# Performance work log

Measured on AMD Instinct MI355X. Metric: run time of the kernel, lower is better.

## Reference

```python
import jax, jax.numpy as jnp
import numpy as np

B, LQ, LK, LKL = 4, 1024, 1024, 512
DX, H, DK = 1024, 16, 64
ALPHA = 0.5
NEG = -1e9
EPS = 1e-5


def setup_inputs() -> dict:
    key = jax.random.key(0)
    ks = jax.random.split(key, 24)
    s = 0.02
    inp = {
        "q": jax.random.normal(ks[0], (B, LQ, DX), jnp.float32),
        "k": jax.random.normal(ks[1], (B, LK, DX), jnp.float32),
        "v": jax.random.normal(ks[2], (B, LK, DX), jnp.float32),
        "kl": jax.random.normal(ks[3], (B, LKL, DX), jnp.float32),
        "vl": jax.random.normal(ks[4], (B, LKL, DX), jnp.float32),
        "pad_mask": jax.random.randint(ks[5], (B, LQ, LK), 0, 2).astype(bool),
        "pad_mask_l": jax.random.randint(ks[6], (B, LQ, LKL), 0, 2).astype(bool),
        "wq_w": jax.random.normal(ks[7], (DX, H * DK), jnp.float32) * s,
        "wq_b": jnp.zeros((H * DK,), jnp.float32),
        "wk_w": jax.random.normal(ks[8], (DX, H * DK), jnp.float32) * s,
        "wk_b": jnp.zeros((H * DK,), jnp.float32),
        "wv_w": jax.random.normal(ks[9], (DX, H * DK), jnp.float32) * s,
        "wv_b": jnp.zeros((H * DK,), jnp.float32),
        "wkl_w": jax.random.normal(ks[10], (DX, H * DK), jnp.float32) * s,
        "wkl_b": jnp.zeros((H * DK,), jnp.float32),
        "wvl_w": jax.random.normal(ks[11], (DX, H * DK), jnp.float32) * s,
        "wvl_b": jnp.zeros((H * DK,), jnp.float32),
        "wo_w": jax.random.normal(ks[12], (H * DK, DX), jnp.float32) * s,
        "wo_b": jnp.zeros((DX,), jnp.float32),
        "ln_g": jnp.ones((DX,), jnp.float32),
        "ln_b": jnp.zeros((DX,), jnp.float32),
    }
    return inp


def _heads(x, w, b, L):
    # (B, L, DX) @ (DX, H*DK) -> (B, H, L, DK)
    y = x @ w + b
    return y.reshape(B, L, H, DK).transpose(0, 2, 1, 3)


def _attn(qh, kh, vh, mask):
    # qh: (B,H,Lq,D), kh/vh: (B,H,Lk,D), mask: (B,Lq,Lk) bool (True = masked)
    scores = jnp.einsum("bhqd,bhkd->bhqk", qh, kh) / np.sqrt(DK).astype(np.float32)
    scores = jnp.where(mask[:, None, :, :], NEG, scores)
    attn = jax.nn.softmax(scores, axis=-1)
    out = jnp.einsum("bhqk,bhkd->bhqd", attn, vh)
    return out, attn


def reference(q, k, v, kl, vl, pad_mask, pad_mask_l,
              wq_w, wq_b, wk_w, wk_b, wv_w, wv_b,
              wkl_w, wkl_b, wvl_w, wvl_b, wo_w, wo_b, ln_g, ln_b):
    X = q
    qh = _heads(q, wq_w, wq_b, LQ)
    kh = _heads(k, wk_w, wk_b, LK)
    vh = _heads(v, wv_w, wv_b, LK)
    klh = _heads(kl, wkl_w, wkl_b, LKL)
    vlh = _heads(vl, wvl_w, wvl_b, LKL)

    out_c, attn_c = _attn(qh, kh, vh, pad_mask)
    out_l, attn_l = _attn(qh, klh, vlh, pad_mask_l)

    out = ALPHA * out_c + (1.0 - ALPHA) * out_l          # (B,H,Lq,DK)
    out = out.transpose(0, 2, 1, 3).reshape(B, LQ, H * DK)
    out = out @ wo_w + wo_b                              # dropout = identity (eval)
    y = out + X
    mu = jnp.mean(y, axis=-1, keepdims=True)
    var = jnp.var(y, axis=-1, keepdims=True)
    y = (y - mu) / jnp.sqrt(var + EPS) * ln_g + ln_b
    return y, attn_c, attn_l
```

## Files before the change

### kernel.cpp

```cpp
#include <hip/hip_runtime.h>
#include <hip/hip_bf16.h>

#define B_   4
#define LQ_  1024
#define LK_  1024
#define LKL_ 512
#define DX_  1024
#define H_   16
#define DK_  64
#define HDK_ 1024
#define NEG_ -1e9f
#define EPS_ 1e-5f

typedef __bf16 bf16_t;
typedef __bf16 bf16x8 __attribute__((ext_vector_type(8)));
typedef __bf16 bf16x4 __attribute__((ext_vector_type(4)));
typedef float  f32x4  __attribute__((ext_vector_type(4)));

__device__ inline f32x4 mfma16(bf16x8 a, bf16x8 b, f32x4 c) {
    return __builtin_amdgcn_mfma_f32_16x16x32_bf16(a, b, c, 0, 0, 0);
}

__device__ __forceinline__ void gload16(const void* g, void* l) {
    __builtin_amdgcn_global_load_lds(
        (const __attribute__((address_space(1))) void*)g,
        (__attribute__((address_space(3))) void*)l, 16, 0, 0);
}

__device__ inline float waveMax(float v) {
#pragma unroll
    for (int o = 32; o > 0; o >>= 1) v = fmaxf(v, __shfl_xor(v, o, 64));
    return v;
}
__device__ inline float waveSum(float v) {
#pragma unroll
    for (int o = 32; o > 0; o >>= 1) v += __shfl_xor(v, o, 64);
    return v;
}

template<int STRIDE>
__device__ inline int sidx(int row, int col) {
    return (row * STRIDE + col) ^ ((row & 15) << 3);
}

__global__ __launch_bounds__(256) void bitpack_mask_kernel(
    const void* __restrict__ mc, const void* __restrict__ ml,
    unsigned long long* __restrict__ bc, unsigned long long* __restrict__ bl)
{
    __shared__ unsigned fl[4];
    {
        const unsigned w = ((const unsigned*)mc)[threadIdx.x];
        const unsigned long long b01 = __ballot(w <= 1u);
        const unsigned long long bfl = __ballot(w == 0u || w == 0x3F800000u);
        if ((threadIdx.x & 63) == 0)
            fl[threadIdx.x >> 6] = ((b01 == ~0ull) ? 1u : 0u) | ((bfl == ~0ull) ? 2u : 0u);
    }
    __syncthreads();
    const unsigned comb = fl[0] & fl[1] & fl[2] & fl[3];
    const unsigned flag = (comb & 1u) ? 0u : ((comb & 2u) ? 2u : 1u);

    const size_t NC = (size_t)B_ * LQ_ * LK_;
    const int lane = threadIdx.x & 63;
    const size_t g = (size_t)blockIdx.x * 256 + threadIdx.x;
    const bool inC = g < NC;
    const size_t idx = inC ? g : g - NC;
    const void* src = inC ? mc : ml;
    bool m;
    if (flag == 0u)      m = ((const int*)src)[idx] != 0;
    else if (flag == 2u) m = ((const float*)src)[idx] != 0.0f;
    else                 m = ((const unsigned char*)src)[idx] != 0;
    const unsigned long long bal = __ballot(m);
    if (lane == 0) {
        unsigned long long* dst = inC ? bc : bl;
        dst[idx >> 6] = bal;
    }
}

struct CvtArgs {
    const float* src[5];
    bf16_t* dst[5];
    int n8[5];
};
__global__ __launch_bounds__(256) void cvt_all_kernel(CvtArgs a)
{
    const int z = blockIdx.y;
    const int i = blockIdx.x * 256 + threadIdx.x;
    if (i >= a.n8[z]) return;
    const float* src = a.src[z];
    const float4 x = ((const float4*)src)[i * 2];
    const float4 y = ((const float4*)src)[i * 2 + 1];
    bf16x8 o;
    o[0] = (bf16_t)x.x; o[1] = (bf16_t)x.y; o[2] = (bf16_t)x.z; o[3] = (bf16_t)x.w;
    o[4] = (bf16_t)y.x; o[5] = (bf16_t)y.y; o[6] = (bf16_t)y.z; o[7] = (bf16_t)y.w;
    ((bf16x8*)a.dst[z])[i] = o;
}

struct WtArgs {
    const float* W[6];
    bf16_t* Wt[6];
};
__global__ __launch_bounds__(256) void wtrans_all_kernel(WtArgs a)
{
    __shared__ float T[64][65];
    const int z = blockIdx.z;
    const float* W = a.W[z];
    bf16_t* Wt = a.Wt[z];
    const int k0 = blockIdx.y * 64, n0 = blockIdx.x * 64;
    const int t = threadIdx.x;
    const int lr = t >> 2, c0 = (t & 3) * 16;
#pragma unroll
    for (int j = 0; j < 4; ++j) {
        const float4 v = *(const float4*)&W[(size_t)(k0 + lr) * DX_ + n0 + c0 + j * 4];
        T[lr][c0 + j * 4 + 0] = v.x; T[lr][c0 + j * 4 + 1] = v.y;
        T[lr][c0 + j * 4 + 2] = v.z; T[lr][c0 + j * 4 + 3] = v.w;
    }
    __syncthreads();
    const int dr = t >> 2;
    bf16x8 o0, o1;
#pragma unroll
    for (int j = 0; j < 8; ++j) {
        o0[j] = (bf16_t)T[c0 + j][dr];
        o1[j] = (bf16_t)T[c0 + 8 + j][dr];
    }
    *(bf16x8*)&Wt[(size_t)(n0 + dr) * DX_ + k0 + c0]     = o0;
    *(bf16x8*)&Wt[(size_t)(n0 + dr) * DX_ + k0 + c0 + 8] = o1;
}

struct TvArgs {
    const bf16_t* V[2];
    bf16_t* Vt[2];
    int L[2];
    int xt[2];
};
__global__ __launch_bounds__(256) void transpose_v_all_kernel(TvArgs a)
{
    __shared__ bf16_t T[64][72];
    const int z = blockIdx.z;
    if ((int)blockIdx.x >= a.xt[z]) return;
    const int L = a.L[z];
    const int bh = blockIdx.y, l0 = blockIdx.x * 64;
    const bf16_t* Vb = a.V[z] + (size_t)bh * L * 64;
    bf16_t* Vtb = a.Vt[z] + (size_t)bh * 64 * L;
    const int t = threadIdx.x;
    {
        const int lr = t >> 2, dc = (t & 3) * 16;
        const bf16x8 x = *(const bf16x8*)&Vb[(size_t)(l0 + lr) * 64 + dc];
        const bf16x8 y = *(const bf16x8*)&Vb[(size_t)(l0 + lr) * 64 + dc + 8];
#pragma unroll
        for (int j = 0; j < 8; ++j) { T[lr][dc + j] = x[j]; T[lr][dc + 8 + j] = y[j]; }
    }
    __syncthreads();
    {
        const int dr = t >> 2, lc = (t & 3) * 16;
        bf16x8 o0, o1;
#pragma unroll
        for (int j = 0; j < 8; ++j) { o0[j] = T[lc + j][dr]; o1[j] = T[lc + 8 + j][dr]; }
        *(bf16x8*)&Vtb[(size_t)dr * L + l0 + lc]     = o0;
        *(bf16x8*)&Vtb[(size_t)dr * L + l0 + lc + 8] = o1;
    }
}

template<int MODE>
__device__ __forceinline__ void gemm2_body(
    const bf16_t* __restrict__ A, const bf16_t* __restrict__ Bt,
    const float* __restrict__ bias,
    void* __restrict__ out, const float* __restrict__ resid, int lshift,
    bf16_t* __restrict__ As, bf16_t* __restrict__ Bs)
{
    char* const AsB = (char*)As;
    char* const BsB = (char*)Bs;
    const int tid = threadIdx.x, wave = tid >> 6, lane = tid & 63;
    const int m0 = blockIdx.y * 128, n0 = blockIdx.x * 128;
    const int wr4 = (wave >> 1) * 32, wc2 = (wave & 1) * 64;

    f32x4 acc[2][4] = {};

    const int srow = wave * 8 + (lane >> 3);
    const int sslot = lane & 7;

    for (int k0 = 0; k0 < 1024; k0 += 64) {
        __syncthreads();
#pragma unroll
        for (int j = 0; j < 2; ++j) {
            const int row = srow + j * 64;
            const int gs = sslot ^ (row & 7);
            gload16(&A[(size_t)(m0 + row) * 1024 + k0 + gs * 8],
                    AsB + j * 8192 + wave * 1024);
            gload16(&Bt[(size_t)(n0 + row) * 1024 + k0 + gs * 8],
                    BsB + j * 8192 + wave * 1024);
        }
        __syncthreads();
#pragma unroll
        for (int kk = 0; kk < 2; ++kk) {
            bf16x8 av[2], bv[4];
#pragma unroll
            for (int i = 0; i < 2; ++i) {
                const int r = wr4 + i * 16 + (lane & 15);
                av[i] = *(const bf16x8*)(AsB + r * 128 + (((kk * 4 + (lane >> 4)) ^ (r & 7)) * 16));
            }
#pragma unroll
            for (int n = 0; n < 4; ++n) {
                const int r = wc2 + n * 16 + (lane & 15);
                bv[n] = *(const bf16x8*)(BsB + r * 128 + (((kk * 4 + (lane >> 4)) ^ (r & 7)) * 16));
            }
#pragma unroll
            for (int i = 0; i < 2; ++i)
#pragma unroll
                for (int n = 0; n < 4; ++n)
                    acc[i][n] = mfma16(av[i], bv[n], acc[i][n]);
        }
    }

#pragma unroll
    for (int i = 0; i < 2; ++i) {
#pragma unroll
        for (int n = 0; n < 4; ++n) {
            const int col = n0 + wc2 + n * 16 + (lane & 15);
            const float bs = bias[col];
            const int row0 = m0 + wr4 + i * 16 + (lane >> 4) * 4;
            if (MODE == 0) {
                const int b = row0 >> lshift, l = row0 & ((1 << lshift) - 1);
                const int h = col >> 6, d = col & 63;
#pragma unroll
                for (int r = 0; r < 4; ++r)
                    ((bf16_t*)out)[(((size_t)(b * H_ + h) << lshift) + l + r) * DK_ + d] =
                        (bf16_t)(acc[i][n][r] + bs);
            } else {
#pragma unroll
                for (int r = 0; r < 4; ++r) {
                    const size_t idx = (size_t)(row0 + r) * DX_ + col;
                    ((float*)out)[idx] = acc[i][n][r] + bs + resid[idx];
                }
            }
        }
    }
}

struct ProjArgs {
    const bf16_t* A[5];
    const bf16_t* Bt[5];
    const float* bias[5];
    bf16_t* out[5];
    int mt[5];
    int lshift[5];
};
__global__ __launch_bounds__(512, 2) void proj_gemm_kernel(ProjArgs a)
{
    __shared__ bf16_t As[128 * 64];
    __shared__ bf16_t Bs[128 * 64];
    const int z = blockIdx.z;
    if ((int)blockIdx.y >= a.mt[z]) return;
    gemm2_body<0>(a.A[z], a.Bt[z], a.bias[z], a.out[z], nullptr, a.lshift[z], As, Bs);
}

__global__ __launch_bounds__(512, 2) void out_gemm_kernel(
    const bf16_t* __restrict__ A, const bf16_t* __restrict__ Bt,
    const float* __restrict__ bias, float* __restrict__ out,
    const float* __restrict__ resid)
{
    __shared__ bf16_t As[128 * 64];
    __shared__ bf16_t Bs[128 * 64];
    gemm2_body<2>(A, Bt, bias, out, resid, 0, As, Bs);
}

template<int LKX, bool COMBINE>
__device__ __forceinline__ void fused_branch_body(
    const bf16_t* __restrict__ Qh, const bf16_t* __restrict__ Kh,
    const bf16_t* __restrict__ Vt, const unsigned* __restrict__ bits,
    float* __restrict__ S, bf16_t* __restrict__ comb,
    bf16_t* __restrict__ Ssh, unsigned* __restrict__ mwords)
{
    const int sid = (blockIdx.x & 7) * 512 + (blockIdx.x >> 3);
    const int bh = sid >> 6, qt = sid & 63;
    const int b = bh >> 4, h = bh & 15;
    const int q0 = qt * 16;
    const int wave = threadIdx.x >> 6, lane = threadIdx.x & 63;
    const int lr = lane & 15, lk8 = (lane >> 4) * 8;
    const int t = threadIdx.x;
    constexpr int WORDS = LKX / 32;

    const bf16_t* Qb  = Qh + (size_t)bh * LQ_ * DK_;
    const bf16_t* Kb  = Kh + (size_t)bh * LKX * DK_;
    const bf16_t* Vtb = Vt + (size_t)bh * DK_ * LKX;
    float* Sout = S + (size_t)bh * LQ_ * LKX;

    for (int w = t; w < 16 * WORDS; w += 256)
        mwords[w] = bits[(size_t)(b * LQ_ + q0) * WORDS + w];

    bf16x8 qf[2];
#pragma unroll
    for (int ks = 0; ks < 2; ++ks)
        qf[ks] = *(const bf16x8*)&Qb[(size_t)(q0 + lr) * DK_ + ks * 32 + lk8];
    __syncthreads();

    constexpr int KTS = LKX / 64;
#pragma unroll
    for (int kt = 0; kt < KTS; ++kt) {
        const int kbase = wave * (LKX / 4) + kt * 16;
        const bf16x8 b0 = *(const bf16x8*)&Kb[(size_t)(kbase + lr) * DK_ + lk8];
        const bf16x8 b1 = *(const bf16x8*)&Kb[(size_t)(kbase + lr) * DK_ + 32 + lk8];
        f32x4 acc = {};
        acc = mfma16(qf[0], b0, acc);
        acc = mfma16(qf[1], b1, acc);
        const int wi = kbase >> 5;
        const int sh = (kbase & 16) + (lane & 15);
#pragma unroll
        for (int r = 0; r < 4; ++r) {
            const int row = (lane >> 4) * 4 + r;
            const bool msk = (mwords[row * WORDS + wi] >> sh) & 1u;
            Ssh[sidx<LKX>(row, kbase + (lane & 15))] = (bf16_t)(msk ? NEG_ : acc[r] * 0.125f);
        }
    }
    __syncthreads();

    constexpr int NP8 = LKX / 512;
#pragma unroll 2
    for (int i = 0; i < 4; ++i) {
        const int row = wave * 4 + i;
        float p[NP8 * 8];
        float m = -INFINITY;
#pragma unroll
        for (int ps = 0; ps < NP8; ++ps) {
            const bf16x8 sv = *(const bf16x8*)&Ssh[sidx<LKX>(row, ps * 512 + lane * 8)];
#pragma unroll
            for (int j = 0; j < 8; ++j) {
                p[ps * 8 + j] = (float)sv[j];
                m = fmaxf(m, p[ps * 8 + j]);
            }
        }
        m = waveMax(m);
        float s = 0.f;
#pragma unroll
        for (int j = 0; j < NP8 * 8; ++j) { p[j] = __expf(p[j] - m); s += p[j]; }
        s = waveSum(s);
        const float inv = 1.f / s;
#pragma unroll
        for (int ps = 0; ps < NP8; ++ps) {
            const int col = ps * 512 + lane * 8;
            bf16x8 pb;
#pragma unroll
            for (int j = 0; j < 8; ++j) pb[j] = (bf16_t)(p[ps * 8 + j] * inv);
            *(bf16x8*)&Ssh[sidx<LKX>(row, col)] = pb;
        }
    }
    __syncthreads();

    f32x4 acc_o = {};
    const int d0 = wave * 16;
#pragma unroll
    for (int ks = 0; ks < LKX / 32; ++ks) {
        const bf16x8 bb = *(const bf16x8*)&Vtb[(size_t)(d0 + lr) * LKX + ks * 32 + lk8];
        const bf16x8 a  = *(const bf16x8*)&Ssh[sidx<LKX>(lr, ks * 32 + lk8)];
        acc_o = mfma16(a, bb, acc_o);
    }

#pragma unroll
    for (int r = 0; r < 4; ++r) {
        const int row = q0 + (lane >> 4) * 4 + r;
        const size_t idx = ((size_t)b * LQ_ + row) * HDK_ + h * DK_ + d0 + (lane & 15);
        const float half = 0.5f * acc_o[r];
        if (COMBINE) comb[idx] = (bf16_t)((float)comb[idx] + half);
        else         comb[idx] = (bf16_t)half;
    }

#pragma unroll
    for (int i = 0; i < 4; ++i) {
        const int row = wave * 4 + i;
        const int rowg = q0 + row;
#pragma unroll
        for (int ps = 0; ps < NP8; ++ps) {
            const int col = ps * 512 + lane * 8;
            const bf16x8 pv8 = *(const bf16x8*)&Ssh[sidx<LKX>(row, col)];
            f32x4 o0, o1;
#pragma unroll
            for (int j = 0; j < 4; ++j) { o0[j] = (float)pv8[j]; o1[j] = (float)pv8[4 + j]; }
            __builtin_nontemporal_store(o0, (f32x4*)&Sout[(size_t)rowg * LKX + col]);
            __builtin_nontemporal_store(o1, (f32x4*)&Sout[(size_t)rowg * LKX + col + 4]);
        }
    }
}

__global__ __launch_bounds__(256, 3) void fused_c_kernel(
    const bf16_t* __restrict__ Qh, const bf16_t* __restrict__ Kh,
    const bf16_t* __restrict__ Vt, const unsigned* __restrict__ bits,
    float* __restrict__ S, bf16_t* __restrict__ comb)
{
    __shared__ bf16_t Ssh[16 * LK_];
    __shared__ unsigned mwords[16 * (LK_ / 32)];
    fused_branch_body<LK_, false>(Qh, Kh, Vt, bits, S, comb, Ssh, mwords);
}

__global__ __launch_bounds__(256, 3) void fused_l_kernel(
    const bf16_t* __restrict__ Qh, const bf16_t* __restrict__ Kh,
    const bf16_t* __restrict__ Vt, const unsigned* __restrict__ bits,
    float* __restrict__ S, bf16_t* __restrict__ comb)
{
    __shared__ bf16_t Ssh[16 * LKL_];
    __shared__ unsigned mwords[16 * (LKL_ / 32)];
    fused_branch_body<LKL_, true>(Qh, Kh, Vt, bits, S, comb, Ssh, mwords);
}

__global__ __launch_bounds__(256) void ln_kernel(
    const float* __restrict__ Y, const float* __restrict__ g,
    const float* __restrict__ be, float* __restrict__ out)
{
    __shared__ float red1[4], red2[4];
    const int tid = threadIdx.x, wave = tid >> 6, lane = tid & 63;
    const float* p = Y + (size_t)blockIdx.x * DX_;
    const float4 x = *(const float4*)&p[tid * 4];
    float s  = x.x + x.y + x.z + x.w;
    float ss = x.x * x.x + x.y * x.y + x.z * x.z + x.w * x.w;
    s = waveSum(s); ss = waveSum(ss);
    if (lane == 0) { red1[wave] = s; red2[wave] = ss; }
    __syncthreads();
    s  = red1[0] + red1[1] + red1[2] + red1[3];
    ss = red2[0] + red2[1] + red2[2] + red2[3];
    const float mean = s * (1.f / DX_);
    const float var  = ss * (1.f / DX_) - mean * mean;
    const float rstd = rsqrtf(var + EPS_);
    const float4 gg = *(const float4*)&g[tid * 4];
    const float4 bb = *(const float4*)&be[tid * 4];
    float4 o;
    o.x = (x.x - mean) * rstd * gg.x + bb.x;
    o.y = (x.y - mean) * rstd * gg.y + bb.y;
    o.z = (x.z - mean) * rstd * gg.z + bb.z;
    o.w = (x.w - mean) * rstd * gg.w + bb.w;
    *(float4*)&out[(size_t)blockIdx.x * DX_ + tid * 4] = o;
}

extern "C" void kernel_launch(void* const* d_in, const int* in_sizes, int n_in,
                              void* d_out, int out_size, void* d_ws, size_t ws_size,
                              hipStream_t stream)
{
    const float* q    = (const float*)d_in[0];
    const float* k    = (const float*)d_in[1];
    const float* v    = (const float*)d_in[2];
    const float* kl   = (const float*)d_in[3];
    const float* vl   = (const float*)d_in[4];
    const void*  mask  = d_in[5];
    const void*  maskl = d_in[6];
    const float* wq_w  = (const float*)d_in[7];
    const float* wq_b  = (const float*)d_in[8];
    const float* wk_w  = (const float*)d_in[9];
    const float* wk_b  = (const float*)d_in[10];
    const float* wv_w  = (const float*)d_in[11];
    const float* wv_b  = (const float*)d_in[12];
    const float* wkl_w = (const float*)d_in[13];
    const float* wkl_b = (const float*)d_in[14];
    const float* wvl_w = (const float*)d_in[15];
    const float* wvl_b = (const float*)d_in[16];
    const float* wo_w  = (const float*)d_in[17];
    const float* wo_b  = (const float*)d_in[18];
    const float* ln_g  = (const float*)d_in[19];
    const float* ln_b  = (const float*)d_in[20];

    char* ws = (char*)d_ws;
    const size_t MiB = 1u << 20;
    bf16_t* qb   = (bf16_t*)(ws);
    bf16_t* kb   = (bf16_t*)(ws +   8 * MiB);
    bf16_t* vb   = (bf16_t*)(ws +  16 * MiB);
    bf16_t* klb  = (bf16_t*)(ws +  24 * MiB);
    bf16_t* vlb  = (bf16_t*)(ws +  28 * MiB);
    bf16_t* qh   = (bf16_t*)(ws +  32 * MiB);
    bf16_t* kh   = (bf16_t*)(ws +  40 * MiB);
    bf16_t* klh  = (bf16_t*)(ws +  48 * MiB);
    bf16_t* vh   = (bf16_t*)(ws +  52 * MiB);
    bf16_t* vlh  = (bf16_t*)(ws +  60 * MiB);
    bf16_t* vt   = (bf16_t*)(ws +  64 * MiB);
    bf16_t* vlt  = (bf16_t*)(ws +  72 * MiB);
    bf16_t* wqT  = (bf16_t*)(ws +  76 * MiB);
    bf16_t* wkT  = (bf16_t*)(ws +  78 * MiB);
    bf16_t* wvT  = (bf16_t*)(ws +  80 * MiB);
    bf16_t* wklT = (bf16_t*)(ws +  82 * MiB);
    bf16_t* wvlT = (bf16_t*)(ws +  84 * MiB);
    bf16_t* woT  = (bf16_t*)(ws +  86 * MiB);
    unsigned long long* bitc = (unsigned long long*)(ws + 89 * MiB);
    unsigned long long* bitl = (unsigned long long*)(ws + 89 * MiB + 512 * 1024);
    bf16_t* comb = (bf16_t*)(ws + 90 * MiB);
    float*  ypre = (float*) (ws);

    float* y_out = (float*)d_out;
    float* Sc = y_out + (size_t)B_ * LQ_ * DX_;
    float* Sl = Sc + (size_t)B_ * H_ * LQ_ * LK_;

    bitpack_mask_kernel<<<dim3((B_*LQ_*(LK_+LKL_)) / 256), 256, 0, stream>>>(
        mask, maskl, bitc, bitl);

    {
        CvtArgs a;
        a.src[0] = q;  a.dst[0] = qb;  a.n8[0] = 524288;
        a.src[1] = k;  a.dst[1] = kb;  a.n8[1] = 524288;
        a.src[2] = v;  a.dst[2] = vb;  a.n8[2] = 524288;
        a.src[3] = kl; a.dst[3] = klb; a.n8[3] = 262144;
        a.src[4] = vl; a.dst[4] = vlb; a.n8[4] = 262144;
        cvt_all_kernel<<<dim3(2048, 5), 256, 0, stream>>>(a);
    }

    {
        WtArgs a;
        a.W[0] = wq_w;  a.Wt[0] = wqT;
        a.W[1] = wk_w;  a.Wt[1] = wkT;
        a.W[2] = wv_w;  a.Wt[2] = wvT;
        a.W[3] = wkl_w; a.Wt[3] = wklT;
        a.W[4] = wvl_w; a.Wt[4] = wvlT;
        a.W[5] = wo_w;  a.Wt[5] = woT;
        wtrans_all_kernel<<<dim3(16, 16, 6), 256, 0, stream>>>(a);
    }

    {
        ProjArgs a;
        a.A[0] = qb;  a.Bt[0] = wqT;  a.bias[0] = wq_b;  a.out[0] = qh;  a.mt[0] = 32; a.lshift[0] = 10;
        a.A[1] = kb;  a.Bt[1] = wkT;  a.bias[1] = wk_b;  a.out[1] = kh;  a.mt[1] = 32; a.lshift[1] = 10;
        a.A[2] = klb; a.Bt[2] = wklT; a.bias[2] = wkl_b; a.out[2] = klh; a.mt[2] = 16; a.lshift[2] = 9;
        a.A[3] = vb;  a.Bt[3] = wvT;  a.bias[3] = wv_b;  a.out[3] = vh;  a.mt[3] = 32; a.lshift[3] = 10;
        a.A[4] = vlb; a.Bt[4] = wvlT; a.bias[4] = wvl_b; a.out[4] = vlh; a.mt[4] = 16; a.lshift[4] = 9;
        proj_gemm_kernel<<<dim3(8, 32, 5), 512, 0, stream>>>(a);
    }

    {
        TvArgs a;
        a.V[0] = vh;  a.Vt[0] = vt;  a.L[0] = LK_;  a.xt[0] = 16;
        a.V[1] = vlh; a.Vt[1] = vlt; a.L[1] = LKL_; a.xt[1] = 8;
        transpose_v_all_kernel<<<dim3(16, 64, 2), 256, 0, stream>>>(a);
    }

    fused_c_kernel<<<dim3(4096), 256, 0, stream>>>(qh, kh,  vt,  (const unsigned*)bitc, Sc, comb);
    fused_l_kernel<<<dim3(4096), 256, 0, stream>>>(qh, klh, vlt, (const unsigned*)bitl, Sl, comb);

    out_gemm_kernel<<<dim3(8, 32), 512, 0, stream>>>(comb, woT, wo_b, ypre, q);

    ln_kernel<<<4096, 256, 0, stream>>>(ypre, ln_g, ln_b, y_out);
}
```

Before: 388.4 us.

## Merge both attention branches into one launch and sum branch outputs in out-GEMM

```diff
diff --git a/kernel.cpp b/kernel.cpp
--- a/kernel.cpp
+++ b/kernel.cpp
@@ -162,7 +162,8 @@
 
 template<int MODE>
 __device__ __forceinline__ void gemm2_body(
-    const bf16_t* __restrict__ A, const bf16_t* __restrict__ Bt,
+    const bf16_t* __restrict__ A, const bf16_t* __restrict__ A2,
+    const bf16_t* __restrict__ Bt,
     const float* __restrict__ bias,
     void* __restrict__ out, const float* __restrict__ resid, int lshift,
     bf16_t* __restrict__ As, bf16_t* __restrict__ Bs)
@@ -184,8 +185,18 @@
         for (int j = 0; j < 2; ++j) {
             const int row = srow + j * 64;
             const int gs = sslot ^ (row & 7);
-            gload16(&A[(size_t)(m0 + row) * 1024 + k0 + gs * 8],
-                    AsB + j * 8192 + wave * 1024);
+            if (MODE == 0) {
+                gload16(&A[(size_t)(m0 + row) * 1024 + k0 + gs * 8],
+                        AsB + j * 8192 + wave * 1024);
+            } else {
+                const bf16x8 ac = *(const bf16x8*)&A [(size_t)(m0 + row) * 1024 + k0 + gs * 8];
+                const bf16x8 al = *(const bf16x8*)&A2[(size_t)(m0 + row) * 1024 + k0 + gs * 8];
+                bf16x8 sum;
+#pragma unroll
+                for (int jj = 0; jj < 8; ++jj)
+                    sum[jj] = (bf16_t)((float)ac[jj] + (float)al[jj]);
+                *(bf16x8*)(AsB + j * 8192 + wave * 1024 + (lane & 63) * 16) = sum;
+            }
             gload16(&Bt[(size_t)(n0 + row) * 1024 + k0 + gs * 8],
                     BsB + j * 8192 + wave * 1024);
         }
@@ -250,33 +261,32 @@
     __shared__ bf16_t Bs[128 * 64];
     const int z = blockIdx.z;
     if ((int)blockIdx.y >= a.mt[z]) return;
-    gemm2_body<0>(a.A[z], a.Bt[z], a.bias[z], a.out[z], nullptr, a.lshift[z], As, Bs);
+    gemm2_body<0>(a.A[z], nullptr, a.Bt[z], a.bias[z], a.out[z], nullptr, a.lshift[z], As, Bs);
 }
 
 __global__ __launch_bounds__(512, 2) void out_gemm_kernel(
-    const bf16_t* __restrict__ A, const bf16_t* __restrict__ Bt,
+    const bf16_t* __restrict__ Ac, const bf16_t* __restrict__ Al,
+    const bf16_t* __restrict__ Bt,
     const float* __restrict__ bias, float* __restrict__ out,
     const float* __restrict__ resid)
 {
     __shared__ bf16_t As[128 * 64];
     __shared__ bf16_t Bs[128 * 64];
-    gemm2_body<2>(A, Bt, bias, out, resid, 0, As, Bs);
-}
-
-template<int LKX, bool COMBINE>
+    gemm2_body<2>(Ac, Al, Bt, bias, out, resid, 0, As, Bs);
+}
+
+template<int LKX>
 __device__ __forceinline__ void fused_branch_body(
     const bf16_t* __restrict__ Qh, const bf16_t* __restrict__ Kh,
     const bf16_t* __restrict__ Vt, const unsigned* __restrict__ bits,
     float* __restrict__ S, bf16_t* __restrict__ comb,
-    bf16_t* __restrict__ Ssh, unsigned* __restrict__ mwords)
-{
-    const int sid = (blockIdx.x & 7) * 512 + (blockIdx.x >> 3);
+    bf16_t* __restrict__ Ssh, int sid)
+{
     const int bh = sid >> 6, qt = sid & 63;
     const int b = bh >> 4, h = bh & 15;
     const int q0 = qt * 16;
     const int wave = threadIdx.x >> 6, lane = threadIdx.x & 63;
     const int lr = lane & 15, lk8 = (lane >> 4) * 8;
-    const int t = threadIdx.x;
     constexpr int WORDS = LKX / 32;
 
     const bf16_t* Qb  = Qh + (size_t)bh * LQ_ * DK_;
@@ -284,14 +294,10 @@
     const bf16_t* Vtb = Vt + (size_t)bh * DK_ * LKX;
     float* Sout = S + (size_t)bh * LQ_ * LKX;
 
-    for (int w = t; w < 16 * WORDS; w += 256)
-        mwords[w] = bits[(size_t)(b * LQ_ + q0) * WORDS + w];
-
     bf16x8 qf[2];
 #pragma unroll
     for (int ks = 0; ks < 2; ++ks)
         qf[ks] = *(const bf16x8*)&Qb[(size_t)(q0 + lr) * DK_ + ks * 32 + lk8];
-    __syncthreads();
 
     constexpr int KTS = LKX / 64;
 #pragma unroll
@@ -307,7 +313,8 @@
 #pragma unroll
         for (int r = 0; r < 4; ++r) {
             const int row = (lane >> 4) * 4 + r;
-            const bool msk = (mwords[row * WORDS + wi] >> sh) & 1u;
+            const unsigned word = bits[(size_t)(b * LQ_ + q0 + row) * WORDS + wi];
+            const bool msk = (word >> sh) & 1u;
             Ssh[sidx<LKX>(row, kbase + (lane & 15))] = (bf16_t)(msk ? NEG_ : acc[r] * 0.125f);
         }
     }
@@ -358,9 +365,7 @@
     for (int r = 0; r < 4; ++r) {
         const int row = q0 + (lane >> 4) * 4 + r;
         const size_t idx = ((size_t)b * LQ_ + row) * HDK_ + h * DK_ + d0 + (lane & 15);
-        const float half = 0.5f * acc_o[r];
-        if (COMBINE) comb[idx] = (bf16_t)((float)comb[idx] + half);
-        else         comb[idx] = (bf16_t)half;
+        comb[idx] = (bf16_t)(0.5f * acc_o[r]);
     }
 
 #pragma unroll
@@ -380,24 +385,24 @@
     }
 }
 
-__global__ __launch_bounds__(256, 3) void fused_c_kernel(
+__global__ __launch_bounds__(256, 3) void fused_attn_all_kernel(
     const bf16_t* __restrict__ Qh, const bf16_t* __restrict__ Kh,
-    const bf16_t* __restrict__ Vt, const unsigned* __restrict__ bits,
-    float* __restrict__ S, bf16_t* __restrict__ comb)
+    const bf16_t* __restrict__ Klh,
+    const bf16_t* __restrict__ Vt, const bf16_t* __restrict__ Vlt,
+    const unsigned* __restrict__ bitc, const unsigned* __restrict__ bitl,
+    float* __restrict__ Sc, float* __restrict__ Sl,
+    bf16_t* __restrict__ comb_c, bf16_t* __restrict__ comb_l)
 {
     __shared__ bf16_t Ssh[16 * LK_];
-    __shared__ unsigned mwords[16 * (LK_ / 32)];
-    fused_branch_body<LK_, false>(Qh, Kh, Vt, bits, S, comb, Ssh, mwords);
-}
-
-__global__ __launch_bounds__(256, 3) void fused_l_kernel(
-    const bf16_t* __restrict__ Qh, const bf16_t* __restrict__ Kh,
-    const bf16_t* __restrict__ Vt, const unsigned* __restrict__ bits,
-    float* __restrict__ S, bf16_t* __restrict__ comb)
-{
-    __shared__ bf16_t Ssh[16 * LKL_];
-    __shared__ unsigned mwords[16 * (LKL_ / 32)];
-    fused_branch_body<LKL_, true>(Qh, Kh, Vt, bits, S, comb, Ssh, mwords);
+    const int bid = blockIdx.x;
+    const int xcd = bid & 7;
+    const int slot = bid >> 3;
+    const int lsel = slot & 1;
+    const int sid = xcd * 512 + (slot >> 1);
+    if (lsel == 0)
+        fused_branch_body<LK_ >(Qh, Kh,  Vt,  bitc, Sc, comb_c, Ssh, sid);
+    else
+        fused_branch_body<LKL_>(Qh, Klh, Vlt, bitl, Sl, comb_l, Ssh, sid);
 }
 
 __global__ __launch_bounds__(256) void ln_kernel(
@@ -476,7 +481,8 @@
     bf16_t* woT  = (bf16_t*)(ws +  86 * MiB);
     unsigned long long* bitc = (unsigned long long*)(ws + 89 * MiB);
     unsigned long long* bitl = (unsigned long long*)(ws + 89 * MiB + 512 * 1024);
-    bf16_t* comb = (bf16_t*)(ws + 90 * MiB);
+    bf16_t* comb_c = (bf16_t*)(ws +  90 * MiB);
+    bf16_t* comb_l = (bf16_t*)(ws +  98 * MiB);
     float*  ypre = (float*) (ws);
 
     float* y_out = (float*)d_out;
@@ -524,10 +530,12 @@
         transpose_v_all_kernel<<<dim3(16, 64, 2), 256, 0, stream>>>(a);
     }
 
-    fused_c_kernel<<<dim3(4096), 256, 0, stream>>>(qh, kh,  vt,  (const unsigned*)bitc, Sc, comb);
-    fused_l_kernel<<<dim3(4096), 256, 0, stream>>>(qh, klh, vlt, (const unsigned*)bitl, Sl, comb);
-
-    out_gemm_kernel<<<dim3(8, 32), 512, 0, stream>>>(comb, woT, wo_b, ypre, q);
+    fused_attn_all_kernel<<<dim3(8192), 256, 0, stream>>>(
+        qh, kh, klh, vt, vlt,
+        (const unsigned*)bitc, (const unsigned*)bitl,
+        Sc, Sl, comb_c, comb_l);
+
+    out_gemm_kernel<<<dim3(8, 32), 512, 0, stream>>>(comb_c, comb_l, woT, wo_b, ypre, q);
 
     ln_kernel<<<4096, 256, 0, stream>>>(ypre, ln_g, ln_b, y_out);
 }
```

Result: slower. 483.9 us (+24.6%).

## Fuse fp32-to-bf16 input conversion into projection GEMM and drop LDS mask staging

Applied to the files above, without the earlier changes.

```diff
diff --git a/kernel.cpp b/kernel.cpp
--- a/kernel.cpp
+++ b/kernel.cpp
@@ -76,25 +76,6 @@
     }
 }
 
-struct CvtArgs {
-    const float* src[5];
-    bf16_t* dst[5];
-    int n8[5];
-};
-__global__ __launch_bounds__(256) void cvt_all_kernel(CvtArgs a)
-{
-    const int z = blockIdx.y;
-    const int i = blockIdx.x * 256 + threadIdx.x;
-    if (i >= a.n8[z]) return;
-    const float* src = a.src[z];
-    const float4 x = ((const float4*)src)[i * 2];
-    const float4 y = ((const float4*)src)[i * 2 + 1];
-    bf16x8 o;
-    o[0] = (bf16_t)x.x; o[1] = (bf16_t)x.y; o[2] = (bf16_t)x.z; o[3] = (bf16_t)x.w;
-    o[4] = (bf16_t)y.x; o[5] = (bf16_t)y.y; o[6] = (bf16_t)y.z; o[7] = (bf16_t)y.w;
-    ((bf16x8*)a.dst[z])[i] = o;
-}
-
 struct WtArgs {
     const float* W[6];
     bf16_t* Wt[6];
@@ -162,7 +143,7 @@
 
 template<int MODE>
 __device__ __forceinline__ void gemm2_body(
-    const bf16_t* __restrict__ A, const bf16_t* __restrict__ Bt,
+    const void* __restrict__ Avoid, const bf16_t* __restrict__ Bt,
     const float* __restrict__ bias,
     void* __restrict__ out, const float* __restrict__ resid, int lshift,
     bf16_t* __restrict__ As, bf16_t* __restrict__ Bs)
@@ -184,8 +165,19 @@
         for (int j = 0; j < 2; ++j) {
             const int row = srow + j * 64;
             const int gs = sslot ^ (row & 7);
-            gload16(&A[(size_t)(m0 + row) * 1024 + k0 + gs * 8],
-                    AsB + j * 8192 + wave * 1024);
+            if (MODE == 0) {
+                const float* Af = (const float*)Avoid;
+                const float4* srcp = (const float4*)&Af[(size_t)(m0 + row) * 1024 + k0 + gs * 8];
+                const float4 xa = srcp[0], xb = srcp[1];
+                bf16x8 t;
+                t[0] = (bf16_t)xa.x; t[1] = (bf16_t)xa.y; t[2] = (bf16_t)xa.z; t[3] = (bf16_t)xa.w;
+                t[4] = (bf16_t)xb.x; t[5] = (bf16_t)xb.y; t[6] = (bf16_t)xb.z; t[7] = (bf16_t)xb.w;
+                *(bf16x8*)(AsB + j * 8192 + wave * 1024 + lane * 16) = t;
+            } else {
+                const bf16_t* Ab = (const bf16_t*)Avoid;
+                gload16(&Ab[(size_t)(m0 + row) * 1024 + k0 + gs * 8],
+                        AsB + j * 8192 + wave * 1024);
+            }
             gload16(&Bt[(size_t)(n0 + row) * 1024 + k0 + gs * 8],
                     BsB + j * 8192 + wave * 1024);
         }
@@ -237,7 +229,7 @@
 }
 
 struct ProjArgs {
-    const bf16_t* A[5];
+    const float* A[5];
     const bf16_t* Bt[5];
     const float* bias[5];
     bf16_t* out[5];
@@ -267,8 +259,7 @@
 __device__ __forceinline__ void fused_branch_body(
     const bf16_t* __restrict__ Qh, const bf16_t* __restrict__ Kh,
     const bf16_t* __restrict__ Vt, const unsigned* __restrict__ bits,
-    float* __restrict__ S, bf16_t* __restrict__ comb,
-    bf16_t* __restrict__ Ssh, unsigned* __restrict__ mwords)
+    float* __restrict__ S, bf16_t* __restrict__ comb, bf16_t* __restrict__ Ssh)
 {
     const int sid = (blockIdx.x & 7) * 512 + (blockIdx.x >> 3);
     const int bh = sid >> 6, qt = sid & 63;
@@ -276,22 +267,24 @@
     const int q0 = qt * 16;
     const int wave = threadIdx.x >> 6, lane = threadIdx.x & 63;
     const int lr = lane & 15, lk8 = (lane >> 4) * 8;
-    const int t = threadIdx.x;
     constexpr int WORDS = LKX / 32;
+    constexpr int WPS   = LKX / 128;
 
     const bf16_t* Qb  = Qh + (size_t)bh * LQ_ * DK_;
     const bf16_t* Kb  = Kh + (size_t)bh * LKX * DK_;
     const bf16_t* Vtb = Vt + (size_t)bh * DK_ * LKX;
     float* Sout = S + (size_t)bh * LQ_ * LKX;
 
-    for (int w = t; w < 16 * WORDS; w += 256)
-        mwords[w] = bits[(size_t)(b * LQ_ + q0) * WORDS + w];
+    const int pwi = wave * WPS + (lane >> 4);
+    const size_t prow_base = (size_t)(b * LQ_ + q0 + (lane & 15)) * WORDS;
+    const unsigned w0 = bits[prow_base + pwi];
+    unsigned w1 = 0;
+    if (WPS == 8) w1 = bits[prow_base + pwi + 4];
 
     bf16x8 qf[2];
 #pragma unroll
     for (int ks = 0; ks < 2; ++ks)
         qf[ks] = *(const bf16x8*)&Qb[(size_t)(q0 + lr) * DK_ + ks * 32 + lk8];
-    __syncthreads();
 
     constexpr int KTS = LKX / 64;
 #pragma unroll
@@ -302,12 +295,14 @@
         f32x4 acc = {};
         acc = mfma16(qf[0], b0, acc);
         acc = mfma16(qf[1], b1, acc);
-        const int wi = kbase >> 5;
+        const int d = kt >> 1;
         const int sh = (kbase & 16) + (lane & 15);
 #pragma unroll
         for (int r = 0; r < 4; ++r) {
             const int row = (lane >> 4) * 4 + r;
-            const bool msk = (mwords[row * WORDS + wi] >> sh) & 1u;
+            const int srcl = row + ((d & 3) << 4);
+            const unsigned word = __shfl((WPS == 8 && d >= 4) ? w1 : w0, srcl, 64);
+            const bool msk = (word >> sh) & 1u;
             Ssh[sidx<LKX>(row, kbase + (lane & 15))] = (bf16_t)(msk ? NEG_ : acc[r] * 0.125f);
         }
     }
@@ -380,24 +375,22 @@
     }
 }
 
-__global__ __launch_bounds__(256, 3) void fused_c_kernel(
+__global__ __launch_bounds__(256, 5) void fused_c_kernel(
     const bf16_t* __restrict__ Qh, const bf16_t* __restrict__ Kh,
     const bf16_t* __restrict__ Vt, const unsigned* __restrict__ bits,
     float* __restrict__ S, bf16_t* __restrict__ comb)
 {
     __shared__ bf16_t Ssh[16 * LK_];
-    __shared__ unsigned mwords[16 * (LK_ / 32)];
-    fused_branch_body<LK_, false>(Qh, Kh, Vt, bits, S, comb, Ssh, mwords);
-}
-
-__global__ __launch_bounds__(256, 3) void fused_l_kernel(
+    fused_branch_body<LK_, false>(Qh, Kh, Vt, bits, S, comb, Ssh);
+}
+
+__global__ __launch_bounds__(256, 5) void fused_l_kernel(
     const bf16_t* __restrict__ Qh, const bf16_t* __restrict__ Kh,
     const bf16_t* __restrict__ Vt, const unsigned* __restrict__ bits,
     float* __restrict__ S, bf16_t* __restrict__ comb)
 {
     __shared__ bf16_t Ssh[16 * LKL_];
-    __shared__ unsigned mwords[16 * (LKL_ / 32)];
-    fused_branch_body<LKL_, true>(Qh, Kh, Vt, bits, S, comb, Ssh, mwords);
+    fused_branch_body<LKL_, true>(Qh, Kh, Vt, bits, S, comb, Ssh);
 }
 
 __global__ __launch_bounds__(256) void ln_kernel(
@@ -456,11 +449,7 @@
 
     char* ws = (char*)d_ws;
     const size_t MiB = 1u << 20;
-    bf16_t* qb   = (bf16_t*)(ws);
-    bf16_t* kb   = (bf16_t*)(ws +   8 * MiB);
-    bf16_t* vb   = (bf16_t*)(ws +  16 * MiB);
-    bf16_t* klb  = (bf16_t*)(ws +  24 * MiB);
-    bf16_t* vlb  = (bf16_t*)(ws +  28 * MiB);
+    float*  ypre = (float*) (ws);
     bf16_t* qh   = (bf16_t*)(ws +  32 * MiB);
     bf16_t* kh   = (bf16_t*)(ws +  40 * MiB);
     bf16_t* klh  = (bf16_t*)(ws +  48 * MiB);
@@ -477,7 +466,6 @@
     unsigned long long* bitc = (unsigned long long*)(ws + 89 * MiB);
     unsigned long long* bitl = (unsigned long long*)(ws + 89 * MiB + 512 * 1024);
     bf16_t* comb = (bf16_t*)(ws + 90 * MiB);
-    float*  ypre = (float*) (ws);
 
     float* y_out = (float*)d_out;
     float* Sc = y_out + (size_t)B_ * LQ_ * DX_;
@@ -485,16 +473,6 @@
 
     bitpack_mask_kernel<<<dim3((B_*LQ_*(LK_+LKL_)) / 256), 256, 0, stream>>>(
         mask, maskl, bitc, bitl);
-
-    {
-        CvtArgs a;
-        a.src[0] = q;  a.dst[0] = qb;  a.n8[0] = 524288;
-        a.src[1] = k;  a.dst[1] = kb;  a.n8[1] = 524288;
-        a.src[2] = v;  a.dst[2] = vb;  a.n8[2] = 524288;
-        a.src[3] = kl; a.dst[3] = klb; a.n8[3] = 262144;
-        a.src[4] = vl; a.dst[4] = vlb; a.n8[4] = 262144;
-        cvt_all_kernel<<<dim3(2048, 5), 256, 0, stream>>>(a);
-    }
 
     {
         WtArgs a;
@@ -509,11 +487,11 @@
 
     {
         ProjArgs a;
-        a.A[0] = qb;  a.Bt[0] = wqT;  a.bias[0] = wq_b;  a.out[0] = qh;  a.mt[0] = 32; a.lshift[0] = 10;
-        a.A[1] = kb;  a.Bt[1] = wkT;  a.bias[1] = wk_b;  a.out[1] = kh;  a.mt[1] = 32; a.lshift[1] = 10;
-        a.A[2] = klb; a.Bt[2] = wklT; a.bias[2] = wkl_b; a.out[2] = klh; a.mt[2] = 16; a.lshift[2] = 9;
-        a.A[3] = vb;  a.Bt[3] = wvT;  a.bias[3] = wv_b;  a.out[3] = vh;  a.mt[3] = 32; a.lshift[3] = 10;
-        a.A[4] = vlb; a.Bt[4] = wvlT; a.bias[4] = wvl_b; a.out[4] = vlh; a.mt[4] = 16; a.lshift[4] = 9;
+        a.A[0] = q;  a.Bt[0] = wqT;  a.bias[0] = wq_b;  a.out[0] = qh;  a.mt[0] = 32; a.lshift[0] = 10;
+        a.A[1] = k;  a.Bt[1] = wkT;  a.bias[1] = wk_b;  a.out[1] = kh;  a.mt[1] = 32; a.lshift[1] = 10;
+        a.A[2] = kl; a.Bt[2] = wklT; a.bias[2] = wkl_b; a.out[2] = klh; a.mt[2] = 16; a.lshift[2] = 9;
+        a.A[3] = v;  a.Bt[3] = wvT;  a.bias[3] = wv_b;  a.out[3] = vh;  a.mt[3] = 32; a.lshift[3] = 10;
+        a.A[4] = vl; a.Bt[4] = wvlT; a.bias[4] = wvl_b; a.out[4] = vlh; a.mt[4] = 16; a.lshift[4] = 9;
         proj_gemm_kernel<<<dim3(8, 32, 5), 512, 0, stream>>>(a);
     }
 
```

Measured after the change: 383.0 us, median of 3. No clear change (-1.4%).
